# Kernel tuning notes

Hardware: AMD Instinct MI355X
Metric: run time of the kernel (lower is better)

The kernel has to match this reference:

```python
import jax, jax.numpy as jnp
import numpy as np

B, V, T, D, NC = 512, 4, 16, 512, 174
EPS = 1e-5
_edges = np.ones((V, V)) - np.eye(V)
SEND = np.where(_edges)[0]   # [12]
RECV = np.where(_edges)[1]   # [12]
E2N = jnp.asarray(np.eye(V)[RECV].T, dtype=jnp.float32)  # [V, E] one-hot recv matrix


def _bn(x, g, b):
    # BatchNorm1d in training mode: batch stats over flattened rows, biased var
    m = x.mean(axis=0)
    v = jnp.var(x, axis=0)
    return (x - m) * jax.lax.rsqrt(v + EPS) * g + b


def _mlp(x, w1, b1, w2, b2, g, bb):
    # RefNRIMLP: Linear-ELU-(Dropout p=0.1 disabled/eval)-Linear-ELU-BN
    h = jax.nn.elu(x @ w1 + b1)
    h = jax.nn.elu(h @ w2 + b2)
    return _bn(h, g, bb)


def setup_inputs() -> dict:
    key = jax.random.key(0)
    ks = iter(jax.random.split(key, 64))
    def W(*s):
        return jax.random.normal(next(ks), s, dtype=jnp.float32) * 0.02
    def zeros(*s):
        return jnp.zeros(s, jnp.float32)
    def ones(*s):
        return jnp.ones(s, jnp.float32)
    return dict(
        global_img_input=zeros(1),
        box_categories=jax.random.randint(next(ks), (B, T, V), 0, 3),
        box_input=jax.random.uniform(next(ks), (B, T, V, 4), dtype=jnp.float32),
        hand_id=jax.random.randint(next(ks), (B,), 0, 2),
        video_label=jax.random.randint(next(ks), (B,), 0, NC),
        emb=W(3, D // 2),
        c2f_w1=W(4, D // 2), c2f_g1=ones(D // 2), c2f_b1=zeros(D // 2),
        c2f_w2=W(D // 2, D), c2f_g2=ones(D), c2f_b2=zeros(D),
        fus_w=W(D + D // 2, D), fus_g=ones(D), fus_b=zeros(D),
        m1_w1=W(2 * D, D), m1_b1=zeros(D), m1_w2=W(D, D), m1_b2=zeros(D), m1_g=ones(D), m1_bb=zeros(D),
        m2_w1=W(D, D), m2_b1=zeros(D), m2_w2=W(D, D), m2_b2=zeros(D), m2_g=ones(D), m2_bb=zeros(D),
        t1_w1=W(2 * D, D), t1_b1=zeros(D), t1_w2=W(D, D), t1_b2=zeros(D), t1_g=ones(D), t1_bb=zeros(D),
        ps_w1=W(D, D), ps_g1=ones(D), ps_b1=zeros(D), ps_w2=W(D, D), ps_g2=ones(D), ps_b2=zeros(D),
        tb_w1=W(T * D, D), tb_g1=ones(D), tb_b1=zeros(D), tb_w2=W(D, D), tb_g2=ones(D), tb_b2=zeros(D),
        cl_w1=W(D, D), cl_b1=zeros(D), cl_w2=W(D, 512), cl_b2=zeros(512),
        cl_w3=W(512, NC), cl_b3=zeros(NC),
    )


def reference(global_img_input, box_categories, box_input, hand_id, video_label,
              emb, c2f_w1, c2f_g1, c2f_b1, c2f_w2, c2f_g2, c2f_b2,
              fus_w, fus_g, fus_b,
              m1_w1, m1_b1, m1_w2, m1_b2, m1_g, m1_bb,
              m2_w1, m2_b1, m2_w2, m2_b2, m2_g, m2_bb,
              t1_w1, t1_b1, t1_w2, t1_b2, t1_g, t1_bb,
              ps_w1, ps_g1, ps_b1, ps_w2, ps_g2, ps_b2,
              tb_w1, tb_g1, tb_b1, tb_w2, tb_g2, tb_b2,
              cl_w1, cl_b1, cl_w2, cl_b2, cl_w3, cl_b3):
    b = hand_id.shape[0]
    # [b,T,V,*] -> [b,V,T,*] -> flatten rows
    x = box_input.transpose(0, 2, 1, 3).reshape(-1, 4)          # [b*V*T, 4]
    cats = box_categories.transpose(0, 2, 1).reshape(-1)        # [b*V*T]
    pad_mask = (jnp.arange(3)[:, None] != 0).astype(emb.dtype)  # padding_idx=0
    ce = (emb * pad_mask)[cats]                                 # [b*V*T, D/2]
    # coord_to_feature: Linear(no bias)-BN-ReLU x2
    h = jax.nn.relu(_bn(x @ c2f_w1, c2f_g1, c2f_b1))
    h = jax.nn.relu(_bn(h @ c2f_w2, c2f_g2, c2f_b2))
    # coord_category_fusion
    bf = jax.nn.relu(_bn(jnp.concatenate([h, ce], axis=1) @ fus_w, fus_g, fus_b))
    bf = bf.reshape(b, V, T, D)
    # node2edge gather + mlp1
    e = jnp.concatenate([bf[:, SEND], bf[:, RECV]], axis=-1).reshape(-1, 2 * D)
    e = _mlp(e, m1_w1, m1_b1, m1_w2, m1_b2, m1_g, m1_bb).reshape(b, len(SEND), T, D)
    # edge2node: one-hot matmul aggregation / (V-1)
    n = jnp.einsum('ve,betd->bvtd', E2N, e) / (V - 1)
    n = _mlp(n.reshape(-1, D), m2_w1, m2_b1, m2_w2, m2_b2, m2_g, m2_bb).reshape(b, V, T, D)
    # temporal MLP on cat(node, bf)
    p = jnp.concatenate([n, bf], axis=-1).reshape(-1, 2 * D)
    p = _mlp(p, t1_w1, t1_b1, t1_w2, t1_b2, t1_g, t1_bb)
    # point_spatial_node_fusion
    p = jax.nn.relu(_bn(p @ ps_w1, ps_g1, ps_b1))
    p = jax.nn.relu(_bn(p @ ps_w2, ps_g2, ps_b2))
    # t_box_feature_fusion over flattened time
    q = p.reshape(b * V, T * D)
    q = jax.nn.relu(_bn(q @ tb_w1, tb_g1, tb_b1))
    q = jax.nn.relu(_bn(q @ tb_w2, tb_g2, tb_b2))
    feat = q.reshape(b, V, D).mean(axis=1)                      # mean over boxes
    h1 = jax.nn.relu(feat @ cl_w1 + cl_b1)
    h2 = jax.nn.relu(h1 @ cl_w2 + cl_b2)
    pf = h2 @ cl_w3 + cl_b3                                      # [b, NC]
    return (pf, video_label)
```

## Files before the change

### kernel.cpp

```cpp
#include <hip/hip_runtime.h>
#include <math.h>

#define EPS_ 1e-5f

static constexpr int Bb = 512, Vv = 4, Tt = 16, Dd = 512, NCc = 174;
static constexpr int NROW = Bb * Vv * Tt;
static constexpr int EROW = Bb * 12 * Tt;
static constexpr int CB = 128;
static constexpr int NCHUNK = Bb / CB;
static constexpr int CROWS_N = CB * Vv * Tt;
static constexpr int CROWS_E = CB * 12 * Tt;

__constant__ int d_SEND[12] = {0,0,0,1,1,1,2,2,2,3,3,3};
__constant__ int d_RECV[12] = {1,2,3,0,2,3,0,1,3,0,1,2};
__constant__ int d_EOFV[4][3] = {{3,6,9},{0,7,10},{1,4,11},{2,5,8}};

typedef float f32x4 __attribute__((ext_vector_type(4)));
typedef short s16x8 __attribute__((ext_vector_type(8)));

static __device__ __forceinline__ float b2f(unsigned short u) {
    union { unsigned int i; float f; } x; x.i = ((unsigned int)u) << 16; return x.f;
}
static __device__ __forceinline__ unsigned short f2b(float f) {
    union { float f; unsigned int i; } x; x.f = f;
    unsigned int r = (x.i + 0x7fffu + ((x.i >> 16) & 1u)) >> 16;
    return (unsigned short)r;
}
static __device__ __forceinline__ float act_f(float v, int act) {
    if (act == 1) return fmaxf(v, 0.f);
    if (act == 2) return (v > 0.f) ? v : (__expf(v) - 1.f);
    return v;
}

#define GL2LDS(g, l) __builtin_amdgcn_global_load_lds(                     \
    (__attribute__((address_space(1))) void*)(g),                          \
    (__attribute__((address_space(3))) void*)(l), 16, 0, 0)

#define CS_STRIDE 136

__global__ __launch_bounds__(256) void gemm_bf16(
    const unsigned short* __restrict__ A0, int Ka0, int K0,
    const unsigned short* __restrict__ A1, int Ka1, int K1,
    const unsigned short* __restrict__ WT, int Kw, int wtoff,
    unsigned short* __restrict__ C, int M, int N,
    const float* __restrict__ bias, int act,
    float* __restrict__ pstats, int accum,
    float* __restrict__ Cpart, int Ksl)
{
    __shared__ __align__(16) unsigned short SMEM[128 * CS_STRIDE];
    unsigned short* As = SMEM;
    unsigned short* Bs = SMEM + 128 * 32;
    int tid = threadIdx.x;
    int lane = tid & 63, wave = tid >> 6;
    int wr = wave >> 1, wc = wave & 1;
    int g = lane >> 4, r16 = lane & 15;

    int nct = N >> 7, nrt = M >> 7;
    int id = blockIdx.x, bx, by;
    if ((nrt & 7) == 0) {
        int grp = id / (nct * 8);
        int rem = id - grp * nct * 8;
        by = grp * 8 + (rem & 7);
        bx = rem >> 3;
    } else { bx = id % nct; by = id / nct; }
    int rowBase = by * 128;
    int colBase = bx * 128;
    int koff = blockIdx.z * Ksl;

    int srow = wave * 32 + (lane >> 2);
    int scol = (lane & 3) * 8;
    unsigned short* lA0 = As + (wave * 32) * 32;
    unsigned short* lA1 = As + (wave * 32 + 16) * 32;
    unsigned short* lB0 = Bs + (wave * 32) * 32;
    unsigned short* lB1 = Bs + (wave * 32 + 16) * 32;
    const unsigned short* wrow  = WT + (size_t)(colBase + srow) * Kw + wtoff + scol;
    const unsigned short* wrow2 = WT + (size_t)(colBase + srow + 16) * Kw + wtoff + scol;

    f32x4 acc[4][4];
#pragma unroll
    for (int i = 0; i < 4; ++i)
#pragma unroll
        for (int j = 0; j < 4; ++j) acc[i][j] = (f32x4){0.f, 0.f, 0.f, 0.f};

    for (int k0 = 0; k0 < Ksl; k0 += 32) {
        int kg = koff + k0;
        const unsigned short* Ap; int lda; int kc;
        if (kg < K0) { Ap = A0; lda = Ka0; kc = kg; }
        else         { Ap = A1; lda = Ka1; kc = kg - K0; }
        const unsigned short* ga = Ap + (size_t)(rowBase + srow) * lda + kc + scol;
        GL2LDS(ga, lA0);
        GL2LDS(ga + (size_t)16 * lda, lA1);
        GL2LDS(wrow + kg, lB0);
        GL2LDS(wrow2 + kg, lB1);
        __syncthreads();
        s16x8 xf[4], wf[4];
#pragma unroll
        for (int j = 0; j < 4; ++j)
            xf[j] = *(const s16x8*)(As + (wr * 64 + j * 16 + r16) * 32 + g * 8);
#pragma unroll
        for (int i = 0; i < 4; ++i)
            wf[i] = *(const s16x8*)(Bs + (wc * 64 + i * 16 + r16) * 32 + g * 8);
#pragma unroll
        for (int i = 0; i < 4; ++i)
#pragma unroll
            for (int j = 0; j < 4; ++j)
                acc[i][j] = __builtin_amdgcn_mfma_f32_16x16x32_bf16(
                    wf[i], xf[j], acc[i][j], 0, 0, 0);
        __syncthreads();
    }

    if (Cpart) {
#pragma unroll
        for (int j = 0; j < 4; ++j) {
            int row = rowBase + wr * 64 + j * 16 + r16;
#pragma unroll
            for (int i = 0; i < 4; ++i) {
                int col0 = colBase + wc * 64 + i * 16 + g * 4;
                float4 v = make_float4(acc[i][j][0], acc[i][j][1],
                                       acc[i][j][2], acc[i][j][3]);
                *(float4*)&Cpart[((size_t)blockIdx.z * M + row) * N + col0] = v;
            }
        }
        return;
    }

#pragma unroll
    for (int i = 0; i < 4; ++i) {
        int lc0 = wc * 64 + i * 16 + g * 4;
        float4 b4 = bias ? *(const float4*)(bias + colBase + lc0)
                         : make_float4(0.f, 0.f, 0.f, 0.f);
        float s[4] = {0.f, 0.f, 0.f, 0.f}, q[4] = {0.f, 0.f, 0.f, 0.f};
#pragma unroll
        for (int j = 0; j < 4; ++j) {
            int lr = wr * 64 + j * 16 + r16;
            float v0 = act_f(acc[i][j][0] + b4.x, act);
            float v1 = act_f(acc[i][j][1] + b4.y, act);
            float v2 = act_f(acc[i][j][2] + b4.z, act);
            float v3 = act_f(acc[i][j][3] + b4.w, act);
            *(ushort4*)&SMEM[lr * CS_STRIDE + lc0] =
                make_ushort4(f2b(v0), f2b(v1), f2b(v2), f2b(v3));
            s[0] += v0; s[1] += v1; s[2] += v2; s[3] += v3;
            q[0] += v0 * v0; q[1] += v1 * v1; q[2] += v2 * v2; q[3] += v3 * v3;
        }
        if (pstats) {
#pragma unroll
            for (int p = 0; p < 4; ++p) {
#pragma unroll
                for (int d = 1; d < 16; d <<= 1) {
                    s[p] += __shfl_xor(s[p], d);
                    q[p] += __shfl_xor(q[p], d);
                }
            }
            if (r16 == 0) {
                float* pr = pstats + ((size_t)(by * 2 + wr)) * 1024 + colBase + lc0;
                float4 s4 = make_float4(s[0], s[1], s[2], s[3]);
                float4 q4 = make_float4(q[0], q[1], q[2], q[3]);
                if (accum) {
                    float4 o = *(float4*)pr;
                    s4.x += o.x; s4.y += o.y; s4.z += o.z; s4.w += o.w;
                    float4 o2 = *(float4*)(pr + 512);
                    q4.x += o2.x; q4.y += o2.y; q4.z += o2.z; q4.w += o2.w;
                }
                *(float4*)pr = s4;
                *(float4*)(pr + 512) = q4;
            }
        }
    }
    __syncthreads();
    {
        int qd = tid & 3;
        int rr = tid >> 2;
#pragma unroll
        for (int pass = 0; pass < 2; ++pass) {
            int lr = pass * 64 + rr;
            size_t grow = (size_t)(rowBase + lr) * N + colBase;
#pragma unroll
            for (int u = 0; u < 4; ++u) {
                int cofs = u * 32 + qd * 8;
                uint4 v = *(const uint4*)(SMEM + lr * CS_STRIDE + cofs);
                *(uint4*)&C[grow + cofs] = v;
            }
        }
    }
}

__global__ __launch_bounds__(256) void finalize_stats_k(
    const float* __restrict__ P, int nrows, float* __restrict__ slot)
{
    __shared__ float red[256];
    int lane = threadIdx.x & 63;
    int seg  = threadIdx.x >> 6;
    int col  = blockIdx.x * 64 + lane;
    float s = 0.f;
    for (int r = seg; r < nrows; r += 4)
        s += P[(size_t)r * 1024 + col];
    red[threadIdx.x] = s;
    __syncthreads();
    if (seg == 0)
        slot[col] = red[lane] + red[64 + lane] + red[128 + lane] + red[192 + lane];
}

__global__ __launch_bounds__(256) void combine_k(
    const float4* __restrict__ P, int S, int M,
    unsigned short* __restrict__ C, float* __restrict__ pstats, int act)
{
    int col4 = threadIdx.x & 127;
    int rh = threadIdx.x >> 7;
    int rb = blockIdx.y * 8;
    float4 s4 = make_float4(0.f, 0.f, 0.f, 0.f);
    float4 q4 = make_float4(0.f, 0.f, 0.f, 0.f);
#pragma unroll
    for (int i = 0; i < 4; ++i) {
        int row = rb + rh + 2 * i;
        float4 v = make_float4(0.f, 0.f, 0.f, 0.f);
#pragma unroll
        for (int z = 0; z < 8; ++z) {
            float4 p = P[((size_t)z * M + row) * 128 + col4];
            v.x += p.x; v.y += p.y; v.z += p.z; v.w += p.w;
        }
        v.x = act_f(v.x, act); v.y = act_f(v.y, act);
        v.z = act_f(v.z, act); v.w = act_f(v.w, act);
        ((ushort4*)C)[(size_t)row * 128 + col4] =
            make_ushort4(f2b(v.x), f2b(v.y), f2b(v.z), f2b(v.w));
        s4.x += v.x; s4.y += v.y; s4.z += v.z; s4.w += v.w;
        q4.x += v.x * v.x; q4.y += v.y * v.y; q4.z += v.z * v.z; q4.w += v.w * v.w;
    }
    __shared__ float4 sb[256], qb[256];
    sb[threadIdx.x] = s4; qb[threadIdx.x] = q4;
    __syncthreads();
    if (threadIdx.x < 128) {
        float4 a = sb[threadIdx.x], b = sb[threadIdx.x + 128];
        float4 c = qb[threadIdx.x], d = qb[threadIdx.x + 128];
        int col = threadIdx.x * 4;
        float* pr = pstats + (size_t)blockIdx.y * 1024 + col;
        *(float4*)pr = make_float4(a.x + b.x, a.y + b.y, a.z + b.z, a.w + b.w);
        *(float4*)(pr + 512) = make_float4(c.x + d.x, c.y + d.y, c.z + d.z, c.w + d.w);
    }
}

#define NTD 13
struct TBatch {
    const float* src[NTD];
    unsigned short* dst[NTD];
    int K[NTD];
    long base[NTD + 1];
};
__global__ __launch_bounds__(256) void transpose_batch_k(TBatch tb, long total)
{
    long i = (long)blockIdx.x * 256 + threadIdx.x;
    if (i >= total) return;
    int d = 0;
#pragma unroll
    for (int j = 0; j < NTD; ++j) if (i >= tb.base[j + 1]) d = j + 1;
    long r = i - tb.base[d];
    int k = (int)(r >> 9), n = (int)(r & 511);
    tb.dst[d][(size_t)n * tb.K[d] + k] = f2b(tb.src[d][r]);
}

__global__ __launch_bounds__(256) void transpose_pq_k(
    const float* __restrict__ W, unsigned short* __restrict__ WT)
{
    int i = blockIdx.x * 256 + threadIdx.x;
    if (i >= 512 * 1024) return;
    int k = i >> 10, n = i & 1023;
    float v = (n < 512) ? W[(size_t)k * 512 + n] : W[(size_t)(512 + k) * 512 + (n - 512)];
    WT[(size_t)n * 512 + k] = f2b(v);
}

__global__ __launch_bounds__(256) void colstats_k(
    const unsigned short* __restrict__ X, float* __restrict__ P)
{
    __shared__ float sb[256][4], qb[256][4];
    int c4 = threadIdx.x & 63;
    int seg = threadIdx.x >> 6;
    int r0 = blockIdx.x * 128;
    float s[4] = {0.f, 0.f, 0.f, 0.f}, q[4] = {0.f, 0.f, 0.f, 0.f};
    for (int r = r0 + seg; r < r0 + 128; r += 4) {
        ushort4 x = ((const ushort4*)X)[(size_t)r * 64 + c4];
        float v0 = b2f(x.x), v1 = b2f(x.y), v2 = b2f(x.z), v3 = b2f(x.w);
        s[0] += v0; s[1] += v1; s[2] += v2; s[3] += v3;
        q[0] += v0 * v0; q[1] += v1 * v1; q[2] += v2 * v2; q[3] += v3 * v3;
    }
#pragma unroll
    for (int e = 0; e < 4; ++e) { sb[threadIdx.x][e] = s[e]; qb[threadIdx.x][e] = q[e]; }
    __syncthreads();
    if (threadIdx.x < 64) {
        int c = threadIdx.x;
        float4 S, Q;
        S.x = sb[c][0] + sb[c + 64][0] + sb[c + 128][0] + sb[c + 192][0];
        S.y = sb[c][1] + sb[c + 64][1] + sb[c + 128][1] + sb[c + 192][1];
        S.z = sb[c][2] + sb[c + 64][2] + sb[c + 128][2] + sb[c + 192][2];
        S.w = sb[c][3] + sb[c + 64][3] + sb[c + 128][3] + sb[c + 192][3];
        Q.x = qb[c][0] + qb[c + 64][0] + qb[c + 128][0] + qb[c + 192][0];
        Q.y = qb[c][1] + qb[c + 64][1] + qb[c + 128][1] + qb[c + 192][1];
        Q.z = qb[c][2] + qb[c + 64][2] + qb[c + 128][2] + qb[c + 192][2];
        Q.w = qb[c][3] + qb[c + 64][3] + qb[c + 128][3] + qb[c + 192][3];
        *(float4*)&P[(size_t)blockIdx.x * 1024 + c * 4] = S;
        *(float4*)&P[(size_t)blockIdx.x * 1024 + 512 + c * 4] = Q;
    }
}

__global__ __launch_bounds__(256) void bn_apply_k(
    unsigned short* __restrict__ X, long n4, int cmask4, int C,
    const float* __restrict__ slot, const float* __restrict__ gm,
    const float* __restrict__ bt, float inv_cnt, float premul, int act)
{
    __shared__ float sc_s[512], sh_s[512];
    for (int c = threadIdx.x; c < C; c += 256) {
        float mean = slot[c] * inv_cnt;
        float var = fmaxf(slot[512 + c] * inv_cnt - mean * mean, 0.f);
        float sc = gm[c] * rsqrtf(var + EPS_);
        sc_s[c] = sc * premul;
        sh_s[c] = bt[c] - mean * sc;
    }
    __syncthreads();
    long stride = (long)gridDim.x * 256;
    for (long i = (long)blockIdx.x * 256 + threadIdx.x; i < n4; i += stride) {
        ushort4 x = ((ushort4*)X)[i];
        int c = ((int)(i & cmask4)) * 4;
        unsigned short o[4] = {x.x, x.y, x.z, x.w};
#pragma unroll
        for (int e = 0; e < 4; ++e) {
            float v = b2f(o[e]) * sc_s[c + e] + sh_s[c + e];
            o[e] = f2b(act_f(v, act));
        }
        ((ushort4*)X)[i] = make_ushort4(o[0], o[1], o[2], o[3]);
    }
}

__global__ __launch_bounds__(256) void zero_k(float* p, int n)
{
    int i = blockIdx.x * 256 + threadIdx.x;
    if (i < n) p[i] = 0.f;
}

__global__ __launch_bounds__(256) void build_x0_k(
    const float* __restrict__ box, float* __restrict__ X0)
{
    int i = blockIdx.x * 256 + threadIdx.x;
    if (i >= NROW * 4) return;
    int c = i & 3; int r = i >> 2;
    int t = r & 15; int bv = r >> 4; int v = bv & 3; int b = bv >> 2;
    X0[i] = box[(((size_t)b * Tt + t) * Vv + v) * 4 + c];
}

__global__ __launch_bounds__(256) void build_ce_k(
    const int* __restrict__ cats, const float* __restrict__ emb,
    unsigned short* __restrict__ CE)
{
    int i = blockIdx.x * 256 + threadIdx.x;
    if (i >= NROW * 64) return;
    int c4 = i & 63; int r = i >> 6;
    int t = r & 15; int bv = r >> 4; int v = bv & 3; int b = bv >> 2;
    int cat = cats[((size_t)b * Tt + t) * Vv + v];
    unsigned short o[4];
#pragma unroll
    for (int e = 0; e < 4; ++e)
        o[e] = (cat == 0) ? 0 : f2b(emb[cat * 256 + c4 * 4 + e]);
    ((ushort4*)CE)[(size_t)r * 64 + c4] = make_ushort4(o[0], o[1], o[2], o[3]);
}

__global__ __launch_bounds__(256) void smallk_gemm_k(
    const float* __restrict__ X0, const float* __restrict__ W4,
    unsigned short* __restrict__ Y1)
{
    int i = blockIdx.x * 256 + threadIdx.x;
    if (i >= NROW * 64) return;
    int n4 = i & 63; int m = i >> 6;
    float4 x = *(const float4*)(X0 + m * 4);
    unsigned short o[4];
#pragma unroll
    for (int e = 0; e < 4; ++e) {
        int n = n4 * 4 + e;
        float v = x.x * W4[n] + x.y * W4[256 + n] + x.z * W4[512 + n] + x.w * W4[768 + n];
        o[e] = f2b(v);
    }
    ((ushort4*)Y1)[(size_t)m * 64 + n4] = make_ushort4(o[0], o[1], o[2], o[3]);
}

__global__ __launch_bounds__(256) void edge_gather_k(
    const unsigned short* __restrict__ PQ,
    const float* __restrict__ b1, unsigned short* __restrict__ E)
{
    int i = blockIdx.x * 256 + threadIdx.x;
    if (i >= CROWS_E * 128) return;
    int c4 = i & 127; int m = i >> 7;
    int t = m & 15; int be = m >> 4; int e = be % 12; int brel = be / 12;
    int s = d_SEND[e], r = d_RECV[e];
    ushort4 p = ((const ushort4*)PQ)[(((size_t)brel * 4 + s) * 16 + t) * 256 + c4];
    ushort4 q = ((const ushort4*)PQ)[(((size_t)brel * 4 + r) * 16 + t) * 256 + 128 + c4];
    unsigned short pa[4] = {p.x, p.y, p.z, p.w}, qa[4] = {q.x, q.y, q.z, q.w}, o[4];
#pragma unroll
    for (int e2 = 0; e2 < 4; ++e2) {
        float v = b2f(pa[e2]) + b2f(qa[e2]) + b1[c4 * 4 + e2];
        o[e2] = f2b(act_f(v, 2));
    }
    ((ushort4*)E)[i] = make_ushort4(o[0], o[1], o[2], o[3]);
}

__global__ __launch_bounds__(256) void edge_agg_k(
    const unsigned short* __restrict__ E2c, unsigned short* __restrict__ nraw, int b0)
{
    int i = blockIdx.x * 256 + threadIdx.x;
    if (i >= CB * Vv * Tt * 128) return;
    int c4 = i & 127; int r = i >> 7;
    int t = r & 15; int r2 = r >> 4; int v = r2 & 3; int brel = r2 >> 2;
    float s[4] = {0.f, 0.f, 0.f, 0.f};
#pragma unroll
    for (int j = 0; j < 3; ++j) {
        int e = d_EOFV[v][j];
        ushort4 x = ((const ushort4*)E2c)[(((size_t)brel * 12 + e) * 16 + t) * 128 + c4];
        s[0] += b2f(x.x); s[1] += b2f(x.y); s[2] += b2f(x.z); s[3] += b2f(x.w);
    }
    ((ushort4*)nraw)[((((size_t)(b0 + brel)) * 4 + v) * 16 + t) * 128 + c4] =
        make_ushort4(f2b(s[0]), f2b(s[1]), f2b(s[2]), f2b(s[3]));
}

__global__ __launch_bounds__(256) void feat_mean_k(
    const unsigned short* __restrict__ q, unsigned short* __restrict__ feat)
{
    int i = blockIdx.x * 256 + threadIdx.x;
    if (i >= Bb * 128) return;
    int c4 = i & 127; int b = i >> 7;
    float s[4] = {0.f, 0.f, 0.f, 0.f};
#pragma unroll
    for (int v = 0; v < 4; ++v) {
        ushort4 x = ((const ushort4*)q)[(((size_t)b * 4 + v)) * 128 + c4];
        s[0] += b2f(x.x); s[1] += b2f(x.y); s[2] += b2f(x.z); s[3] += b2f(x.w);
    }
    ((ushort4*)feat)[(size_t)b * 128 + c4] = make_ushort4(
        f2b(0.25f * s[0]), f2b(0.25f * s[1]), f2b(0.25f * s[2]), f2b(0.25f * s[3]));
}

__global__ __launch_bounds__(256) void final_gemm_k(
    const unsigned short* __restrict__ H2, const float* __restrict__ W,
    const float* __restrict__ b, float* __restrict__ out)
{
    int i = blockIdx.x * 256 + threadIdx.x;
    if (i >= Bb * NCc) return;
    int n = i % NCc; int m = i / NCc;
    float s = b[n];
    for (int k = 0; k < 512; ++k)
        s += b2f(H2[(size_t)m * 512 + k]) * W[(size_t)k * NCc + n];
    out[i] = s;
}

__global__ __launch_bounds__(256) void copy_labels_k(
    const int* __restrict__ lab, float* __restrict__ out)
{
    int i = blockIdx.x * 256 + threadIdx.x;
    if (i < Bb) out[i] = (float)lab[i];
}

static inline void gemm(hipStream_t s,
                        const unsigned short* A0, int Ka0, int K0,
                        const unsigned short* A1, int Ka1, int K1,
                        const unsigned short* WT, int Kw, int wtoff,
                        unsigned short* C, int M, int N,
                        const float* bias, int act, float* pstats, int accum)
{
    dim3 g((N / 128) * (M / 128), 1, 1);
    hipLaunchKernelGGL(gemm_bf16, g, dim3(256), 0, s,
                       A0, Ka0, K0, A1, Ka1, K1, WT, Kw, wtoff, C, M, N,
                       bias, act, pstats, accum, (float*)nullptr, K0 + K1);
}

static inline void finalize(hipStream_t s, const float* P, int nrows, float* slot)
{
    hipLaunchKernelGGL(finalize_stats_k, dim3(16), dim3(256), 0, s, P, nrows, slot);
}

static inline void bn_apply(hipStream_t s, unsigned short* X, long n, int C,
                            const float* slot, const float* gm, const float* bt,
                            float cnt, float premul, int act)
{
    long n4 = n / 4;
    long nb = (n4 + 255) / 256;
    if (nb > 1024) nb = 1024;
    hipLaunchKernelGGL(bn_apply_k, dim3((unsigned)nb), dim3(256), 0, s,
                       X, n4, C / 4 - 1, C, slot, gm, bt, 1.f / cnt, premul, act);
}

extern "C" void kernel_launch(void* const* d_in, const int* in_sizes, int n_in,
                              void* d_out, int out_size, void* d_ws, size_t ws_size,
                              hipStream_t stream)
{
    const int*   box_cat = (const int*)  d_in[1];
    const float* box_in  = (const float*)d_in[2];
    const int*   vlabel  = (const int*)  d_in[4];
    const float* emb     = (const float*)d_in[5];
    const float* c2f_w1  = (const float*)d_in[6];
    const float* c2f_g1  = (const float*)d_in[7];
    const float* c2f_b1  = (const float*)d_in[8];
    const float* c2f_w2  = (const float*)d_in[9];
    const float* c2f_g2  = (const float*)d_in[10];
    const float* c2f_b2  = (const float*)d_in[11];
    const float* fus_w   = (const float*)d_in[12];
    const float* fus_g   = (const float*)d_in[13];
    const float* fus_b   = (const float*)d_in[14];
    const float* m1_w1   = (const float*)d_in[15];
    const float* m1_b1   = (const float*)d_in[16];
    const float* m1_w2   = (const float*)d_in[17];
    const float* m1_b2   = (const float*)d_in[18];
    const float* m1_g    = (const float*)d_in[19];
    const float* m1_bb   = (const float*)d_in[20];
    const float* m2_w1   = (const float*)d_in[21];
    const float* m2_b1   = (const float*)d_in[22];
    const float* m2_w2   = (const float*)d_in[23];
    const float* m2_b2   = (const float*)d_in[24];
    const float* m2_g    = (const float*)d_in[25];
    const float* m2_bb   = (const float*)d_in[26];
    const float* t1_w1   = (const float*)d_in[27];
    const float* t1_b1   = (const float*)d_in[28];
    const float* t1_w2   = (const float*)d_in[29];
    const float* t1_b2   = (const float*)d_in[30];
    const float* t1_g    = (const float*)d_in[31];
    const float* t1_bb   = (const float*)d_in[32];
    const float* ps_w1   = (const float*)d_in[33];
    const float* ps_g1   = (const float*)d_in[34];
    const float* ps_b1   = (const float*)d_in[35];
    const float* ps_w2   = (const float*)d_in[36];
    const float* ps_g2   = (const float*)d_in[37];
    const float* ps_b2   = (const float*)d_in[38];
    const float* tb_w1   = (const float*)d_in[39];
    const float* tb_g1   = (const float*)d_in[40];
    const float* tb_b1   = (const float*)d_in[41];
    const float* tb_w2   = (const float*)d_in[42];
    const float* tb_g2   = (const float*)d_in[43];
    const float* tb_b2   = (const float*)d_in[44];
    const float* cl_w1   = (const float*)d_in[45];
    const float* cl_b1   = (const float*)d_in[46];
    const float* cl_w2   = (const float*)d_in[47];
    const float* cl_b2   = (const float*)d_in[48];
    const float* cl_w3   = (const float*)d_in[49];
    const float* cl_b3   = (const float*)d_in[50];

    float* out = (float*)d_out;

    char* base = (char*)d_ws;
    const size_t SZ_ACT = (size_t)NROW * 512 * 2;
    unsigned short* A0v = (unsigned short*)(base);
    unsigned short* A1v = (unsigned short*)(base + SZ_ACT);
    char* Sreg = base + 2 * SZ_ACT;
    unsigned short* A2v = (unsigned short*)Sreg;
    unsigned short* CE  = (unsigned short*)Sreg;
    unsigned short* Y1  = (unsigned short*)(Sreg + (size_t)NROW * 256 * 2);
    unsigned short* PQc = (unsigned short*)Sreg;
    unsigned short* EC1 = (unsigned short*)(Sreg + (size_t)CROWS_N * 1024 * 2);
    unsigned short* EC2 = (unsigned short*)(Sreg + (size_t)CROWS_N * 1024 * 2
                                                 + (size_t)CROWS_E * 512 * 2);
    float* Ppart = (float*)Sreg;
    char* wtb = Sreg + (size_t)CROWS_N * 1024 * 2 + 2 * (size_t)CROWS_E * 512 * 2;
    unsigned short* wtp = (unsigned short*)wtb;
    size_t wo = 0;
    auto alloc_wt = [&](int K) { unsigned short* p = wtp + wo; wo += (size_t)K * 512; return p; };
    unsigned short* WTc2f2 = alloc_wt(256);
    unsigned short* WTfus  = alloc_wt(768);
    unsigned short* WTpq   = alloc_wt(1024);
    unsigned short* WTm1b  = alloc_wt(512);
    unsigned short* WTm2a  = alloc_wt(512);
    unsigned short* WTm2b  = alloc_wt(512);
    unsigned short* WTt1a  = alloc_wt(1024);
    unsigned short* WTt1b  = alloc_wt(512);
    unsigned short* WTps1  = alloc_wt(512);
    unsigned short* WTps2  = alloc_wt(512);
    unsigned short* WTtb1  = alloc_wt(8192);
    unsigned short* WTtb2  = alloc_wt(512);
    unsigned short* WTcl1  = alloc_wt(512);
    unsigned short* WTcl2  = alloc_wt(512);
    float* X0f    = (float*)(wtp + wo);
    float* STATS  = X0f + (size_t)NROW * 4;
    float* PSTATS = STATS + 10 * 1024;

    auto slot = [&](int i) { return STATS + (size_t)i * 1024; };

    {
        int nz = 10 * 1024 + 384 * 1024;
        hipLaunchKernelGGL(zero_k, dim3((nz + 255) / 256), dim3(256), 0, stream,
                           STATS, nz);
    }
    {
        TBatch tb;
        const float* srcs[NTD] = {c2f_w2, fus_w, m1_w2, m2_w1, m2_w2, t1_w1, t1_w2,
                                  ps_w1, ps_w2, tb_w1, tb_w2, cl_w1, cl_w2};
        unsigned short* dsts[NTD] = {WTc2f2, WTfus, WTm1b, WTm2a, WTm2b, WTt1a, WTt1b,
                                     WTps1, WTps2, WTtb1, WTtb2, WTcl1, WTcl2};
        int Ks[NTD] = {256, 768, 512, 512, 512, 1024, 512, 512, 512, 8192, 512, 512, 512};
        long acc = 0;
        for (int i = 0; i < NTD; ++i) {
            tb.src[i] = srcs[i]; tb.dst[i] = dsts[i]; tb.K[i] = Ks[i];
            tb.base[i] = acc; acc += (long)Ks[i] * 512;
        }
        tb.base[NTD] = acc;
        hipLaunchKernelGGL(transpose_batch_k, dim3((unsigned)((acc + 255) / 256)),
                           dim3(256), 0, stream, tb, acc);
    }
    hipLaunchKernelGGL(transpose_pq_k, dim3((512 * 1024 + 255) / 256), dim3(256), 0,
                       stream, m1_w1, WTpq);

    hipLaunchKernelGGL(build_x0_k, dim3((NROW * 4 + 255) / 256), dim3(256), 0, stream,
                       box_in, X0f);
    hipLaunchKernelGGL(build_ce_k, dim3((NROW * 64 + 255) / 256), dim3(256), 0, stream,
                       box_cat, emb, CE);

    hipLaunchKernelGGL(smallk_gemm_k, dim3((NROW * 64 + 255) / 256), dim3(256), 0,
                       stream, X0f, c2f_w1, Y1);
    hipLaunchKernelGGL(colstats_k, dim3(NROW / 128), dim3(256), 0, stream, Y1, PSTATS);
    finalize(stream, PSTATS, NROW / 128, slot(0));
    bn_apply(stream, Y1, (long)NROW * 256, 256, slot(0), c2f_g1, c2f_b1,
             (float)NROW, 1.f, 1);

    gemm(stream, Y1, 256, 256, nullptr, 0, 0, WTc2f2, 256, 0, A1v, NROW, 512,
         nullptr, 0, PSTATS, 0);
    finalize(stream, PSTATS, 512, slot(1));
    bn_apply(stream, A1v, (long)NROW * 512, 512, slot(1), c2f_g2, c2f_b2,
             (float)NROW, 1.f, 1);

    gemm(stream, A1v, 512, 512, CE, 256, 256, WTfus, 768, 0, A0v, NROW, 512,
         nullptr, 0, PSTATS, 0);
    finalize(stream, PSTATS, 512, slot(2));
    bn_apply(stream, A0v, (long)NROW * 512, 512, slot(2), fus_g, fus_b,
             (float)NROW, 1.f, 1);

    for (int c = 0; c < NCHUNK; ++c) {
        const unsigned short* BFc = A0v + (size_t)c * CROWS_N * 512;
        gemm(stream, BFc, 512, 512, nullptr, 0, 0, WTpq, 512, 0, PQc, CROWS_N, 1024,
             nullptr, 0, nullptr, 0);
        hipLaunchKernelGGL(edge_gather_k, dim3((CROWS_E * 128 + 255) / 256), dim3(256),
                           0, stream, PQc, m1_b1, EC1);
        gemm(stream, EC1, 512, 512, nullptr, 0, 0, WTm1b, 512, 0, EC2, CROWS_E, 512,
             m1_b2, 2, PSTATS, 1);
        hipLaunchKernelGGL(edge_agg_k, dim3((CB * Vv * Tt * 128 + 255) / 256), dim3(256),
                           0, stream, EC2, A1v, c * CB);
    }
    finalize(stream, PSTATS, 384, slot(3));
    bn_apply(stream, A1v, (long)NROW * 512, 512, slot(3), m1_g, m1_bb,
             (float)EROW, 1.f / 3.f, 0);

    gemm(stream, A1v, 512, 512, nullptr, 0, 0, WTm2a, 512, 0, A2v, NROW, 512,
         m2_b1, 2, nullptr, 0);
    gemm(stream, A2v, 512, 512, nullptr, 0, 0, WTm2b, 512, 0, A1v, NROW, 512,
         m2_b2, 2, PSTATS, 0);
    finalize(stream, PSTATS, 512, slot(4));
    bn_apply(stream, A1v, (long)NROW * 512, 512, slot(4), m2_g, m2_bb,
             (float)NROW, 1.f, 0);

    gemm(stream, A1v, 512, 512, A0v, 512, 512, WTt1a, 1024, 0, A2v, NROW, 512,
         t1_b1, 2, nullptr, 0);
    gemm(stream, A2v, 512, 512, nullptr, 0, 0, WTt1b, 512, 0, A1v, NROW, 512,
         t1_b2, 2, PSTATS, 0);
    finalize(stream, PSTATS, 512, slot(5));
    bn_apply(stream, A1v, (long)NROW * 512, 512, slot(5), t1_g, t1_bb,
             (float)NROW, 1.f, 0);

    gemm(stream, A1v, 512, 512, nullptr, 0, 0, WTps1, 512, 0, A2v, NROW, 512,
         nullptr, 0, PSTATS, 0);
    finalize(stream, PSTATS, 512, slot(6));
    bn_apply(stream, A2v, (long)NROW * 512, 512, slot(6), ps_g1, ps_b1,
             (float)NROW, 1.f, 1);

    gemm(stream, A2v, 512, 512, nullptr, 0, 0, WTps2, 512, 0, A0v, NROW, 512,
         nullptr, 0, PSTATS, 0);
    finalize(stream, PSTATS, 512, slot(7));
    bn_apply(stream, A0v, (long)NROW * 512, 512, slot(7), ps_g2, ps_b2,
             (float)NROW, 1.f, 1);

    {
        dim3 g((512 / 128) * (2048 / 128), 1, 8);
        hipLaunchKernelGGL(gemm_bf16, g, dim3(256), 0, stream,
                           A0v, 8192, 8192, (const unsigned short*)nullptr, 0, 0,
                           WTtb1, 8192, 0, A1v, 2048, 512,
                           (const float*)nullptr, 0, (float*)nullptr, 0, Ppart, 1024);
        hipLaunchKernelGGL(combine_k, dim3(1, 2048 / 8), dim3(256), 0, stream,
                           (const float4*)Ppart, 8, 2048, A1v, PSTATS, 0);
        finalize(stream, PSTATS, 2048 / 8, slot(8));
    }
    bn_apply(stream, A1v, (long)Bb * Vv * 512, 512, slot(8), tb_g1, tb_b1,
             (float)(Bb * Vv), 1.f, 1);

    gemm(stream, A1v, 512, 512, nullptr, 0, 0, WTtb2, 512, 0, A2v, Bb * Vv, 512,
         nullptr, 0, PSTATS, 0);
    finalize(stream, PSTATS, (Bb * Vv / 128) * 2, slot(9));
    bn_apply(stream, A2v, (long)Bb * Vv * 512, 512, slot(9), tb_g2, tb_b2,
             (float)(Bb * Vv), 1.f, 1);

    hipLaunchKernelGGL(feat_mean_k, dim3((Bb * 128 + 255) / 256), dim3(256), 0, stream,
                       A2v, A0v);

    gemm(stream, A0v, 512, 512, nullptr, 0, 0, WTcl1, 512, 0, A1v, Bb, 512,
         cl_b1, 1, nullptr, 0);
    gemm(stream, A1v, 512, 512, nullptr, 0, 0, WTcl2, 512, 0, A2v, Bb, 512,
         cl_b2, 1, nullptr, 0);
    hipLaunchKernelGGL(final_gemm_k, dim3((Bb * NCc + 255) / 256), dim3(256), 0, stream,
                       A2v, cl_w3, cl_b3, out);

    hipLaunchKernelGGL(copy_labels_k, dim3((Bb + 255) / 256), dim3(256), 0, stream,
                       vlabel, out + (size_t)Bb * NCc);
}
```

Measured before the change: 1.467 ms.

## Double-buffer LDS tiles in bf16 GEMM to overlap loads with MFMA

Splits shared memory into two A/B tile buffers and issues the global-to-LDS loads for the next k-tile before computing on the current one. The main loop now has a single barrier per iteration instead of two. This aims to hide global load latency behind MFMA work. It relies on the existing end-of-iteration barrier for correctness and may increase register or LDS pressure slightly.

```diff
diff --git a/kernel.cpp b/kernel.cpp
--- a/kernel.cpp
+++ b/kernel.cpp
@@ -48,8 +48,10 @@
     float* __restrict__ Cpart, int Ksl)
 {
     __shared__ __align__(16) unsigned short SMEM[128 * CS_STRIDE];
-    unsigned short* As = SMEM;
-    unsigned short* Bs = SMEM + 128 * 32;
+    unsigned short* SA0 = SMEM;
+    unsigned short* SB0 = SMEM + 4096;
+    unsigned short* SA1 = SMEM + 8192;
+    unsigned short* SB1 = SMEM + 12288;
     int tid = threadIdx.x;
     int lane = tid & 63, wave = tid >> 6;
     int wr = wave >> 1, wc = wave & 1;
@@ -69,10 +71,6 @@
 
     int srow = wave * 32 + (lane >> 2);
     int scol = (lane & 3) * 8;
-    unsigned short* lA0 = As + (wave * 32) * 32;
-    unsigned short* lA1 = As + (wave * 32 + 16) * 32;
-    unsigned short* lB0 = Bs + (wave * 32) * 32;
-    unsigned short* lB1 = Bs + (wave * 32 + 16) * 32;
     const unsigned short* wrow  = WT + (size_t)(colBase + srow) * Kw + wtoff + scol;
     const unsigned short* wrow2 = WT + (size_t)(colBase + srow + 16) * Kw + wtoff + scol;
 
@@ -82,24 +80,36 @@
 #pragma unroll
         for (int j = 0; j < 4; ++j) acc[i][j] = (f32x4){0.f, 0.f, 0.f, 0.f};
 
-    for (int k0 = 0; k0 < Ksl; k0 += 32) {
-        int kg = koff + k0;
-        const unsigned short* Ap; int lda; int kc;
-        if (kg < K0) { Ap = A0; lda = Ka0; kc = kg; }
-        else         { Ap = A1; lda = Ka1; kc = kg - K0; }
-        const unsigned short* ga = Ap + (size_t)(rowBase + srow) * lda + kc + scol;
-        GL2LDS(ga, lA0);
-        GL2LDS(ga + (size_t)16 * lda, lA1);
-        GL2LDS(wrow + kg, lB0);
-        GL2LDS(wrow2 + kg, lB1);
-        __syncthreads();
+#define STAGE_(kg_, SA_, SB_) do {                                              \
+        int kg = (kg_);                                                         \
+        const unsigned short* Ap; int lda; int kc;                              \
+        if (kg < K0) { Ap = A0; lda = Ka0; kc = kg; }                           \
+        else         { Ap = A1; lda = Ka1; kc = kg - K0; }                      \
+        const unsigned short* ga = Ap + (size_t)(rowBase + srow) * lda + kc + scol; \
+        GL2LDS(ga, (SA_) + wave * 1024);                                        \
+        GL2LDS(ga + (size_t)16 * lda, (SA_) + wave * 1024 + 512);               \
+        GL2LDS(wrow + kg, (SB_) + wave * 1024);                                 \
+        GL2LDS(wrow2 + kg, (SB_) + wave * 1024 + 512);                          \
+    } while (0)
+
+    int nt = Ksl >> 5;
+    STAGE_(koff, SA0, SB0);
+    __syncthreads();
+    for (int t = 0; t < nt; ++t) {
+        unsigned short* SA = (t & 1) ? SA1 : SA0;
+        unsigned short* SB = (t & 1) ? SB1 : SB0;
+        if (t + 1 < nt) {
+            unsigned short* PA = (t & 1) ? SA0 : SA1;
+            unsigned short* PB = (t & 1) ? SB0 : SB1;
+            STAGE_(koff + (t + 1) * 32, PA, PB);
+        }
         s16x8 xf[4], wf[4];
 #pragma unroll
         for (int j = 0; j < 4; ++j)
-            xf[j] = *(const s16x8*)(As + (wr * 64 + j * 16 + r16) * 32 + g * 8);
+            xf[j] = *(const s16x8*)(SA + (wr * 64 + j * 16 + r16) * 32 + g * 8);
 #pragma unroll
         for (int i = 0; i < 4; ++i)
-            wf[i] = *(const s16x8*)(Bs + (wc * 64 + i * 16 + r16) * 32 + g * 8);
+            wf[i] = *(const s16x8*)(SB + (wc * 64 + i * 16 + r16) * 32 + g * 8);
 #pragma unroll
         for (int i = 0; i < 4; ++i)
 #pragma unroll
@@ -108,6 +118,7 @@
                     wf[i], xf[j], acc[i][j], 0, 0, 0);
         __syncthreads();
     }
+#undef STAGE_
 
     if (Cpart) {
 #pragma unroll
```

Measured after the change: 1.335 ms. -9.0%, faster.
